# Kernel optimization log

Measured on AMD Instinct MI355X. Metric: run time of the kernel, lower is better.

The kernel has to match this reference:

```python
import jax, jax.numpy as jnp
import numpy as np

SEQ, HID = 4096, 1024
NEG_INF = -10000000000.0


def setup_inputs() -> dict:
    key = jax.random.key(0)
    ks = jax.random.split(key, 6)
    s = 1.0 / np.sqrt(HID)
    return {
        "query": jax.random.normal(ks[0], (SEQ, HID), jnp.float32),
        "key": jax.random.normal(ks[1], (SEQ, HID), jnp.float32),
        "value": jax.random.normal(ks[2], (SEQ, HID), jnp.float32),
        # SASRec causal mask: allowed positions are 1, masked are 0
        "mask": jnp.tril(jnp.ones((SEQ, SEQ), jnp.int32)),
        "Wq": jax.random.normal(ks[3], (HID, HID), jnp.float32) * s,
        "Wk": jax.random.normal(ks[4], (HID, HID), jnp.float32) * s,
        "Wv": jax.random.normal(ks[5], (HID, HID), jnp.float32) * s,
    }


def reference(query, key, value, mask, Wq, Wk, Wv):
    # nn.Linear(bias=False): y = x @ W.T
    Q = query @ Wq.T   # [S, H]
    K = key @ Wk.T     # [S, H]
    V = value @ Wv.T   # [S, H]
    scale = jnp.sqrt(jnp.asarray(HID, Q.dtype))
    energy = (Q @ K.T) / scale                      # [S, S]
    energy = jnp.where(mask == 0, NEG_INF, energy)  # masked_fill
    attention = jax.nn.softmax(energy, axis=-1)     # [S, S]
    x = attention @ V                               # dropout is identity in eval
    return (x, attention)
```

## Files before the change

### kernel.cpp

```cpp
#include <hip/hip_runtime.h>

#define SEQ 4096
#define HID 1024

typedef _Float16 f16x4 __attribute__((ext_vector_type(4)));
typedef _Float16 f16x8 __attribute__((ext_vector_type(8)));
typedef float    f32x4 __attribute__((ext_vector_type(4)));

__device__ __forceinline__ void gld16(const void* g, void* l) {
    __builtin_amdgcn_global_load_lds(
        (const __attribute__((address_space(1))) unsigned int*)g,
        (__attribute__((address_space(3))) unsigned int*)l, 16, 0, 0);
}

__global__ __launch_bounds__(256) void cast_all(
    const float4* __restrict__ q, const float4* __restrict__ k,
    const float4* __restrict__ v,
    const float4* __restrict__ wq, const float4* __restrict__ wk,
    const float4* __restrict__ wv,
    f16x4* __restrict__ qh, f16x4* __restrict__ kh, f16x4* __restrict__ vh,
    f16x4* __restrict__ wqh, f16x4* __restrict__ wkh, f16x4* __restrict__ wvh,
    int nX4, int nW4) {
    int t = blockIdx.x * 256 + threadIdx.x;
    const float4 *a, *b, *c; f16x4 *da, *db, *dc; int idx;
    if (t < nX4) { a = q; b = k; c = v; da = qh; db = kh; dc = vh; idx = t; }
    else if (t < nX4 + nW4) {
        idx = t - nX4;
        a = wq; b = wk; c = wv; da = wqh; db = wkh; dc = wvh;
    } else return;
    float4 va = a[idx], vb = b[idx], vc = c[idx];
    f16x4 oa = {(_Float16)va.x, (_Float16)va.y, (_Float16)va.z, (_Float16)va.w};
    f16x4 ob = {(_Float16)vb.x, (_Float16)vb.y, (_Float16)vb.z, (_Float16)vb.w};
    f16x4 oc = {(_Float16)vc.x, (_Float16)vc.y, (_Float16)vc.z, (_Float16)vc.w};
    da[idx] = oa; db[idx] = ob; dc[idx] = oc;
}

__global__ __launch_bounds__(256) void transpose_f16(
    const _Float16* __restrict__ src, _Float16* __restrict__ dst,
    int R, int C) {
    __shared__ _Float16 tile[32][33];
    int c0 = blockIdx.x * 32, r0 = blockIdx.y * 32;
    int tr = threadIdx.x >> 5, tc = threadIdx.x & 31;
#pragma unroll
    for (int q = 0; q < 4; ++q)
        tile[tr + q * 8][tc] = src[(size_t)(r0 + tr + q * 8) * C + c0 + tc];
    __syncthreads();
#pragma unroll
    for (int q = 0; q < 4; ++q)
        dst[(size_t)(c0 + tr + q * 8) * R + r0 + tc] = tile[tc][tr + q * 8];
}

template <typename OutT, bool TRI_SKIP, bool TRI_K, int ZMODE>
__global__ __launch_bounds__(256) void gemm_nt(
    const _Float16* __restrict__ A, const _Float16* __restrict__ Bt,
    OutT* __restrict__ C, int M, int N, int K, float scale,
    long sA, long sB, long sC, int KC, float* __restrict__ PB) {
    __shared__ __attribute__((aligned(16))) _Float16 As[2 * 128 * 32];
    __shared__ __attribute__((aligned(16))) _Float16 Bs[2 * 128 * 32];

    int bm = blockIdx.y;
    const int bn = blockIdx.x;
    if (TRI_SKIP && bn > bm) return;
    if (ZMODE == 1) {
        A  += (long)blockIdx.z * sA;
        Bt += (long)blockIdx.z * sB;
        C  += (long)blockIdx.z * sC;
    }

    int kstart = 0, kend, zslot = -1;
    if (ZMODE == 4) {
        const int y = 79 - (int)blockIdx.y;
        int g = 0;
        while (4 * (g + 1) * (g + 2) <= y) ++g;
        const int rem = y - 4 * g * (g + 1);
        const int m   = g + 1;
        const int rg  = rem / m;
        bm = 8 * g + rg;
        const int z = rem - rg * m;
        kstart = z * KC;
        kend   = min((bm + 1) * 128, kstart + KC);
        if (z > 0) zslot = 4 * g * (g - 1) + rg * g + (z - 1);
    } else {
        kend = TRI_K ? min(K, (bm + 1) * 128) : K;
    }

    const int tid = threadIdx.x;
    const int tr  = tid >> 2;
    const int tc8 = (tid & 3) * 8;

    const _Float16* Ab = A  + (size_t)bm * 128 * K;
    const _Float16* Bb = Bt + (size_t)bn * 128 * K;

    const int wave = tid >> 6;
    const int lane = tid & 63;
    const int wm = (wave >> 1) * 64;
    const int wn = (wave & 1) * 64;
    const int lr = lane & 15;
    const int lk = (lane >> 4) * 8;

    f32x4 acc[4][4];
#pragma unroll
    for (int i = 0; i < 4; ++i)
#pragma unroll
        for (int j = 0; j < 4; ++j) acc[i][j] = (f32x4)0.0f;

    for (int k0 = kstart; k0 < kend; k0 += 64) {
#pragma unroll
        for (int h = 0; h < 2; ++h) {
            const int kk = k0 + h * 32, off = h * 4096;
            gld16(Ab + (size_t)tr * K        + kk + tc8, &As[off + tr * 32 + tc8]);
            gld16(Ab + (size_t)(64 + tr) * K + kk + tc8, &As[off + (64 + tr) * 32 + tc8]);
            gld16(Bb + (size_t)tr * K        + kk + tc8, &Bs[off + tr * 32 + tc8]);
            gld16(Bb + (size_t)(64 + tr) * K + kk + tc8, &Bs[off + (64 + tr) * 32 + tc8]);
        }
        __syncthreads();

#pragma unroll
        for (int h = 0; h < 2; ++h) {
            const int off = h * 4096;
            f16x8 af[4], bfr[4];
#pragma unroll
            for (int i = 0; i < 4; ++i)
                af[i] = *(const f16x8*)&As[off + (wm + i * 16 + lr) * 32 + lk];
#pragma unroll
            for (int j = 0; j < 4; ++j)
                bfr[j] = *(const f16x8*)&Bs[off + (wn + j * 16 + lr) * 32 + lk];
#pragma unroll
            for (int i = 0; i < 4; ++i)
#pragma unroll
                for (int j = 0; j < 4; ++j)
                    acc[i][j] = __builtin_amdgcn_mfma_f32_16x16x32_f16(
                        af[i], bfr[j], acc[i][j], 0, 0, 0);
        }
        __syncthreads();
    }

    const int er = (lane >> 4) * 4;
    const int ec = lane & 15;
#pragma unroll
    for (int i = 0; i < 4; ++i) {
#pragma unroll
        for (int j = 0; j < 4; ++j) {
            const int lrow0 = wm + i * 16 + er;
            const int col   = bn * 128 + wn + j * 16 + ec;
#pragma unroll
            for (int r = 0; r < 4; ++r) {
                const float val = acc[i][j][r] * scale;
                if (ZMODE == 4 && zslot >= 0)
                    PB[(size_t)(zslot * 128 + lrow0 + r) * 1024 + col] = val;
                else
                    C[(size_t)(bm * 128 + lrow0 + r) * N + col] = (OutT)val;
            }
        }
    }
}

__global__ __launch_bounds__(256) void reduce_pv(
    float* __restrict__ out, const float* __restrict__ PB) {
    const int row = 1024 + blockIdx.x;
    const int bm  = row >> 7;
    const int g   = bm >> 3;
    const int slot0 = 4 * g * (g - 1) + (bm - 8 * g) * g;
    const int rloc  = row & 127;
    float4* o = (float4*)(out + (size_t)row * 1024) + threadIdx.x;
    float4 acc = *o;
    for (int z = 0; z < g; ++z) {
        const float4 p = *((const float4*)(PB +
            ((size_t)(slot0 + z) * 128 + rloc) * 1024) + threadIdx.x);
        acc.x += p.x; acc.y += p.y; acc.z += p.z; acc.w += p.w;
    }
    *o = acc;
}

__global__ __launch_bounds__(256) void softmax_causal(
    _Float16* __restrict__ EP, float* __restrict__ att, int S) {
    __shared__ float rowbuf[SEQ];
    __shared__ float red[8];
    const int i   = blockIdx.x;
    const int tid = threadIdx.x;
    const int wv  = tid >> 6, ln = tid & 63;
    _Float16* Erow = EP + (size_t)i * S;

    float lmax = -INFINITY;
    for (int j8 = tid * 8; j8 <= i; j8 += 2048) {
        f16x8 e8 = *(const f16x8*)&Erow[j8];
#pragma unroll
        for (int u = 0; u < 8; ++u) {
            int j = j8 + u;
            if (j <= i) {
                float vv = (float)e8[u];
                rowbuf[j] = vv;
                lmax = fmaxf(lmax, vv);
            }
        }
    }
#pragma unroll
    for (int o = 32; o > 0; o >>= 1) lmax = fmaxf(lmax, __shfl_down(lmax, o, 64));
    if (ln == 0) red[wv] = lmax;
    __syncthreads();
    if (tid == 0)
        red[4] = fmaxf(fmaxf(red[0], red[1]), fmaxf(red[2], red[3]));
    __syncthreads();
    const float rmax = red[4];

    float lsum = 0.0f;
    for (int j4 = tid * 4; j4 <= i; j4 += 1024) {
        float4 e = *(float4*)&rowbuf[j4];
        float4 o;
        o.x = (j4     <= i) ? __expf(e.x - rmax) : 0.f;
        o.y = (j4 + 1 <= i) ? __expf(e.y - rmax) : 0.f;
        o.z = (j4 + 2 <= i) ? __expf(e.z - rmax) : 0.f;
        o.w = (j4 + 3 <= i) ? __expf(e.w - rmax) : 0.f;
        *(float4*)&rowbuf[j4] = o;
        lsum += o.x + o.y + o.z + o.w;
    }
#pragma unroll
    for (int o = 32; o > 0; o >>= 1) lsum += __shfl_down(lsum, o, 64);
    __syncthreads();
    if (ln == 0) red[wv] = lsum;
    __syncthreads();
    if (tid == 0)
        red[4] = red[0] + red[1] + red[2] + red[3];
    __syncthreads();
    const float rinv = 1.0f / red[4];

    float* arow = att + (size_t)i * S;
    const int jlim = ((i >> 7) + 1) << 7;
    for (int j4 = tid * 4; j4 < S; j4 += 1024) {
        float4 a;
        a.x = (j4     <= i) ? rowbuf[j4]     * rinv : 0.f;
        a.y = (j4 + 1 <= i) ? rowbuf[j4 + 1] * rinv : 0.f;
        a.z = (j4 + 2 <= i) ? rowbuf[j4 + 2] * rinv : 0.f;
        a.w = (j4 + 3 <= i) ? rowbuf[j4 + 3] * rinv : 0.f;
        *(float4*)&arow[j4] = a;
        if (j4 < jlim) {
            f16x4 p = {(_Float16)a.x, (_Float16)a.y, (_Float16)a.z, (_Float16)a.w};
            *(f16x4*)&Erow[j4] = p;
        }
    }
}

extern "C" void kernel_launch(void* const* d_in, const int* in_sizes, int n_in,
                              void* d_out, int out_size, void* d_ws, size_t ws_size,
                              hipStream_t stream) {
    const float* q  = (const float*)d_in[0];
    const float* k  = (const float*)d_in[1];
    const float* v  = (const float*)d_in[2];
    const float* Wq = (const float*)d_in[4];
    const float* Wk = (const float*)d_in[5];
    const float* Wv = (const float*)d_in[6];

    float* out_x   = (float*)d_out;
    float* out_att = out_x + (size_t)SEQ * HID;

    char* ws = (char*)d_ws;
    const size_t SH = (size_t)SEQ * HID * sizeof(_Float16);
    const size_t HH = (size_t)HID * HID * sizeof(_Float16);
    _Float16* qh  = (_Float16*)(ws);
    _Float16* kh  = (_Float16*)(ws + SH);
    _Float16* vh  = (_Float16*)(ws + 2 * SH);
    _Float16* wqh = (_Float16*)(ws + 3 * SH);
    _Float16* wkh = (_Float16*)(ws + 3 * SH + HH);
    _Float16* wvh = (_Float16*)(ws + 3 * SH + 2 * HH);
    _Float16* Mt  = (_Float16*)(ws + 3 * SH + 3 * HH);
    _Float16* WqT = (_Float16*)(ws + 3 * SH + 4 * HH);
    _Float16* WkT = (_Float16*)(ws + 3 * SH + 5 * HH);
    _Float16* Qh  = (_Float16*)(ws + 3 * SH + 6 * HH);
    _Float16* Vh  = (_Float16*)(ws + 5 * SH + 6 * HH);
    _Float16* VT  = (_Float16*)(ws + 6 * SH + 6 * HH);
    _Float16* EP  = (_Float16*)(ws + 7 * SH + 6 * HH);
    float* Pbuf = (float*)ws;

    const int nX4 = SEQ * HID / 4, nW4 = HID * HID / 4;
    cast_all<<<(nX4 + nW4 + 255) / 256, 256, 0, stream>>>(
        (const float4*)q, (const float4*)k, (const float4*)v,
        (const float4*)Wq, (const float4*)Wk, (const float4*)Wv,
        (f16x4*)qh, (f16x4*)kh, (f16x4*)vh,
        (f16x4*)wqh, (f16x4*)wkh, (f16x4*)wvh, nX4, nW4);

    transpose_f16<<<dim3(HID / 32, HID / 32), 256, 0, stream>>>(wqh, WqT, HID, HID);
    transpose_f16<<<dim3(HID / 32, HID / 32), 256, 0, stream>>>(wkh, WkT, HID, HID);
    gemm_nt<_Float16, false, false, 0><<<dim3(HID / 128, HID / 128), 256, 0, stream>>>(
        WkT, WqT, Mt, HID, HID, HID, 1.0f, 0, 0, 0, 0, nullptr);

    gemm_nt<_Float16, false, false, 1><<<dim3(HID / 128, SEQ / 128, 2), 256, 0, stream>>>(
        qh, Mt, Qh, SEQ, HID, HID, 1.0f,
        (long)(2 * SEQ * HID), (long)(wvh - Mt), (long)(2 * SEQ * HID), 0, nullptr);

    transpose_f16<<<dim3(HID / 32, SEQ / 32), 256, 0, stream>>>(Vh, VT, SEQ, HID);

    gemm_nt<_Float16, true, false, 0><<<dim3(SEQ / 128, SEQ / 128), 256, 0, stream>>>(
        Qh, kh, EP, SEQ, SEQ, HID, 0.03125f, 0, 0, 0, 0, nullptr);

    softmax_causal<<<SEQ, 256, 0, stream>>>(EP, out_att, SEQ);

    gemm_nt<float, false, true, 4><<<dim3(HID / 128, 80), 256, 0, stream>>>(
        EP, VT, out_x, SEQ, HID, SEQ, 1.0f, 0, 0, 0, 1024, Pbuf);

    reduce_pv<<<3072, 256, 0, stream>>>(out_x, Pbuf);
}
```

Measured before the change: 324.7 us.

## Split-K the causal QK^T GEMM and fuse V projection into transposed output

Computes the V projection directly in transposed form inside the same launch as the Q·M projection, eliminating a separate transpose kernel. Splits the triangular QK^T GEMM into two K halves writing fp16 partials, and sums them in the softmax, so more blocks are available to fill the GPU. This adds an extra partial-buffer read in softmax and an extra fp16 rounding of partial energies.

```diff
diff --git a/kernel.cpp b/kernel.cpp
--- a/kernel.cpp
+++ b/kernel.cpp
@@ -54,17 +54,23 @@
 __global__ __launch_bounds__(256) void gemm_nt(
     const _Float16* __restrict__ A, const _Float16* __restrict__ Bt,
     OutT* __restrict__ C, int M, int N, int K, float scale,
-    long sA, long sB, long sC, int KC, float* __restrict__ PB) {
+    long sA, long sB, long sC, int KC, float* __restrict__ PB,
+    const _Float16* __restrict__ A2, const _Float16* __restrict__ B2,
+    OutT* __restrict__ C2, int N2) {
     __shared__ __attribute__((aligned(16))) _Float16 As[2 * 128 * 32];
     __shared__ __attribute__((aligned(16))) _Float16 Bs[2 * 128 * 32];
 
     int bm = blockIdx.y;
-    const int bn = blockIdx.x;
+    int bn = blockIdx.x;
     if (TRI_SKIP && bn > bm) return;
-    if (ZMODE == 1) {
-        A  += (long)blockIdx.z * sA;
-        Bt += (long)blockIdx.z * sB;
-        C  += (long)blockIdx.z * sC;
+    const _Float16* Ap = A;
+    const _Float16* Bp = Bt;
+    OutT* Cp = C;
+    int Nloc = N;
+    if (ZMODE == 6 && blockIdx.y >= 32) {
+        const int lin = (blockIdx.y - 32) * 8 + blockIdx.x;
+        bm = lin >> 5; bn = lin & 31;
+        Ap = A2; Bp = B2; Cp = C2; Nloc = N2;
     }
 
     int kstart = 0, kend, zslot = -1;
@@ -80,6 +86,10 @@
         kstart = z * KC;
         kend   = min((bm + 1) * 128, kstart + KC);
         if (z > 0) zslot = 4 * g * (g - 1) + rg * g + (z - 1);
+    } else if (ZMODE == 5) {
+        kstart = blockIdx.z * KC;
+        kend   = kstart + KC;
+        Cp += (long)blockIdx.z * sC;
     } else {
         kend = TRI_K ? min(K, (bm + 1) * 128) : K;
     }
@@ -88,8 +98,8 @@
     const int tr  = tid >> 2;
     const int tc8 = (tid & 3) * 8;
 
-    const _Float16* Ab = A  + (size_t)bm * 128 * K;
-    const _Float16* Bb = Bt + (size_t)bn * 128 * K;
+    const _Float16* Ab = Ap + (size_t)bm * 128 * K;
+    const _Float16* Bb = Bp + (size_t)bn * 128 * K;
 
     const int wave = tid >> 6;
     const int lane = tid & 63;
@@ -149,7 +159,7 @@
                 if (ZMODE == 4 && zslot >= 0)
                     PB[(size_t)(zslot * 128 + lrow0 + r) * 1024 + col] = val;
                 else
-                    C[(size_t)(bm * 128 + lrow0 + r) * N + col] = (OutT)val;
+                    Cp[(long)(bm * 128 + lrow0 + r) * Nloc + col] = (OutT)val;
             }
         }
     }
@@ -173,22 +183,25 @@
 }
 
 __global__ __launch_bounds__(256) void softmax_causal(
-    _Float16* __restrict__ EP, float* __restrict__ att, int S) {
+    _Float16* __restrict__ EP0, const _Float16* __restrict__ EP1,
+    float* __restrict__ att, int S) {
     __shared__ float rowbuf[SEQ];
     __shared__ float red[8];
     const int i   = blockIdx.x;
     const int tid = threadIdx.x;
     const int wv  = tid >> 6, ln = tid & 63;
-    _Float16* Erow = EP + (size_t)i * S;
+    _Float16* E0row = EP0 + (size_t)i * S;
+    const _Float16* E1row = EP1 + (size_t)i * S;
 
     float lmax = -INFINITY;
     for (int j8 = tid * 8; j8 <= i; j8 += 2048) {
-        f16x8 e8 = *(const f16x8*)&Erow[j8];
+        f16x8 a8 = *(const f16x8*)&E0row[j8];
+        f16x8 b8 = *(const f16x8*)&E1row[j8];
 #pragma unroll
         for (int u = 0; u < 8; ++u) {
             int j = j8 + u;
             if (j <= i) {
-                float vv = (float)e8[u];
+                float vv = (float)a8[u] + (float)b8[u];
                 rowbuf[j] = vv;
                 lmax = fmaxf(lmax, vv);
             }
@@ -235,7 +248,7 @@
         *(float4*)&arow[j4] = a;
         if (j4 < jlim) {
             f16x4 p = {(_Float16)a.x, (_Float16)a.y, (_Float16)a.z, (_Float16)a.w};
-            *(f16x4*)&Erow[j4] = p;
+            *(f16x4*)&E0row[j4] = p;
         }
     }
 }
@@ -257,18 +270,18 @@
     const size_t SH = (size_t)SEQ * HID * sizeof(_Float16);
     const size_t HH = (size_t)HID * HID * sizeof(_Float16);
     _Float16* qh  = (_Float16*)(ws);
-    _Float16* kh  = (_Float16*)(ws + SH);
-    _Float16* vh  = (_Float16*)(ws + 2 * SH);
-    _Float16* wqh = (_Float16*)(ws + 3 * SH);
-    _Float16* wkh = (_Float16*)(ws + 3 * SH + HH);
-    _Float16* wvh = (_Float16*)(ws + 3 * SH + 2 * HH);
-    _Float16* Mt  = (_Float16*)(ws + 3 * SH + 3 * HH);
-    _Float16* WqT = (_Float16*)(ws + 3 * SH + 4 * HH);
-    _Float16* WkT = (_Float16*)(ws + 3 * SH + 5 * HH);
-    _Float16* Qh  = (_Float16*)(ws + 3 * SH + 6 * HH);
-    _Float16* Vh  = (_Float16*)(ws + 5 * SH + 6 * HH);
-    _Float16* VT  = (_Float16*)(ws + 6 * SH + 6 * HH);
-    _Float16* EP  = (_Float16*)(ws + 7 * SH + 6 * HH);
+    _Float16* vh  = (_Float16*)(ws + SH);
+    _Float16* wqh = (_Float16*)(ws + 2 * SH);
+    _Float16* wkh = (_Float16*)(ws + 2 * SH + HH);
+    _Float16* wvh = (_Float16*)(ws + 2 * SH + 2 * HH);
+    _Float16* WqT = (_Float16*)(ws + 2 * SH + 3 * HH);
+    _Float16* WkT = (_Float16*)(ws + 2 * SH + 4 * HH);
+    _Float16* Mt  = (_Float16*)(ws + 2 * SH + 5 * HH);
+    _Float16* EP1 = (_Float16*)(ws);
+    _Float16* kh  = (_Float16*)(ws + 4 * SH);
+    _Float16* Qh  = (_Float16*)(ws + 5 * SH);
+    _Float16* VT  = (_Float16*)(ws + 6 * SH);
+    _Float16* EP0 = (_Float16*)(ws + 7 * SH);
     float* Pbuf = (float*)ws;
 
     const int nX4 = SEQ * HID / 4, nW4 = HID * HID / 4;
@@ -281,21 +294,22 @@
     transpose_f16<<<dim3(HID / 32, HID / 32), 256, 0, stream>>>(wqh, WqT, HID, HID);
     transpose_f16<<<dim3(HID / 32, HID / 32), 256, 0, stream>>>(wkh, WkT, HID, HID);
     gemm_nt<_Float16, false, false, 0><<<dim3(HID / 128, HID / 128), 256, 0, stream>>>(
-        WkT, WqT, Mt, HID, HID, HID, 1.0f, 0, 0, 0, 0, nullptr);
-
-    gemm_nt<_Float16, false, false, 1><<<dim3(HID / 128, SEQ / 128, 2), 256, 0, stream>>>(
-        qh, Mt, Qh, SEQ, HID, HID, 1.0f,
-        (long)(2 * SEQ * HID), (long)(wvh - Mt), (long)(2 * SEQ * HID), 0, nullptr);
-
-    transpose_f16<<<dim3(HID / 32, SEQ / 32), 256, 0, stream>>>(Vh, VT, SEQ, HID);
-
-    gemm_nt<_Float16, true, false, 0><<<dim3(SEQ / 128, SEQ / 128), 256, 0, stream>>>(
-        Qh, kh, EP, SEQ, SEQ, HID, 0.03125f, 0, 0, 0, 0, nullptr);
-
-    softmax_causal<<<SEQ, 256, 0, stream>>>(EP, out_att, SEQ);
+        WkT, WqT, Mt, HID, HID, HID, 1.0f, 0, 0, 0, 0, nullptr,
+        nullptr, nullptr, nullptr, 0);
+
+    gemm_nt<_Float16, false, false, 6><<<dim3(8, 64), 256, 0, stream>>>(
+        qh, Mt, Qh, SEQ, HID, HID, 1.0f, 0, 0, 0, 0, nullptr,
+        wvh, vh, VT, SEQ);
+
+    gemm_nt<_Float16, true, false, 5><<<dim3(SEQ / 128, SEQ / 128, 2), 256, 0, stream>>>(
+        Qh, kh, EP0, SEQ, SEQ, HID, 0.03125f,
+        0, 0, (long)(EP1 - EP0), 512, nullptr, nullptr, nullptr, nullptr, 0);
+
+    softmax_causal<<<SEQ, 256, 0, stream>>>(EP0, EP1, out_att, SEQ);
 
     gemm_nt<float, false, true, 4><<<dim3(HID / 128, 80), 256, 0, stream>>>(
-        EP, VT, out_x, SEQ, HID, SEQ, 1.0f, 0, 0, 0, 1024, Pbuf);
+        EP0, VT, out_x, SEQ, HID, SEQ, 1.0f, 0, 0, 0, 1024, Pbuf,
+        nullptr, nullptr, nullptr, 0);
 
     reduce_pv<<<3072, 256, 0, stream>>>(out_x, Pbuf);
 }
```

Result: faster. 318.2 us (-2.0%).
